# Optimization experiments

Hardware: AMD Instinct MI355X
Metric: run time of the kernel (lower is better)

## Reference

```python
import jax, jax.numpy as jnp
import numpy as np

SOFTCAP = 50.0
EPS = 1e-6
N_HEADS, D_HEAD = 16, 64


def _rms(x, w):
    return x * jax.lax.rsqrt(jnp.mean(x * x, axis=-1, keepdims=True) + EPS) * w


def _rope(x, cos, sin):
    # Faithful to source: apply_rope uses x.size(1) as the position axis, but is
    # called on (B, H, T, Dh) tensors, so positions are indexed by HEAD index.
    n = x.shape[1]
    x1, x2 = x[..., 0::2], x[..., 1::2]
    c = cos[:n][None, :, None, :]
    s = sin[:n][None, :, None, :]
    return jnp.stack([x1 * c - x2 * s, x1 * s + x2 * c], axis=-1).reshape(x.shape)


def setup_inputs() -> dict:
    key = jax.random.key(0)
    ks = jax.random.split(key, 12)
    L, D, H, Dh, Dff, V, B, T = 6, 1024, N_HEADS, D_HEAD, 4096, 32000, 1, 1024
    r = lambda k, shape: jax.random.normal(k, shape, dtype=jnp.float32) * 0.02
    return {
        'x': jax.random.randint(ks[0], (B, T), 0, V, dtype=jnp.int32),
        'embed': r(ks[1], (V, D)),
        'ln1': jnp.ones((L, D), jnp.float32),
        'Wq': r(ks[2], (L, H * Dh, D)),
        'Wk': r(ks[3], (L, H * Dh, D)),
        'Wv': r(ks[4], (L, H * Dh, D)),
        'Wo': r(ks[5], (L, D, H * Dh)),
        'qn': jnp.ones((L, Dh), jnp.float32),
        'kn': jnp.ones((L, Dh), jnp.float32),
        'ln2': jnp.ones((L, D), jnp.float32),
        'Wg': r(ks[6], (L, Dff, D)),
        'Wu': r(ks[7], (L, Dff, D)),
        'Wd': r(ks[8], (L, D, Dff)),
        'ln_out': jnp.ones((D,), jnp.float32),
    }


def reference(x, embed, ln1, Wq, Wk, Wv, Wo, qn, kn, ln2, Wg, Wu, Wd, ln_out):
    B, T = x.shape
    H, Dh = N_HEADS, D_HEAD
    scale = Dh ** -0.5
    # RoPE tables (theta=10000)
    freqs = 1.0 / (10000.0 ** (jnp.arange(0, Dh, 2, dtype=jnp.float32) / Dh))
    ang = jnp.arange(T, dtype=jnp.float32)[:, None] * freqs[None, :]
    cos, sin = jnp.cos(ang), jnp.sin(ang)
    mask = jnp.triu(jnp.ones((T, T), dtype=bool), k=1)  # True above diagonal

    h = embed[x]  # (B, T, D)

    def block(h, p):
        l1, wq, wk, wv, wo, qnw, knw, l2, wg, wu, wd = p
        hn = _rms(h, l1)
        q = (hn @ wq.T).reshape(B, T, H, Dh).transpose(0, 2, 1, 3)  # (B,H,T,Dh)
        k = (hn @ wk.T).reshape(B, T, H, Dh).transpose(0, 2, 1, 3)
        v = (hn @ wv.T).reshape(B, T, H, Dh).transpose(0, 2, 1, 3)
        q = _rope(_rms(q, qnw), cos, sin)
        k = _rope(_rms(k, knw), cos, sin)
        scores = jnp.einsum('bhtd,bhsd->bhts', q, k) * scale
        scores = SOFTCAP * jnp.tanh(scores / SOFTCAP)
        scores = jnp.where(mask[None, None], -jnp.inf, scores)
        attn = jax.nn.softmax(scores, axis=-1)
        o = jnp.einsum('bhts,bhsd->bhtd', attn, v)
        o = o.transpose(0, 2, 1, 3).reshape(B, T, H * Dh)
        h = h + o @ wo.T
        hn2 = _rms(h, l2)
        h = h + (jax.nn.silu(hn2 @ wg.T) * (hn2 @ wu.T)) @ wd.T
        return h, None

    h, _ = jax.lax.scan(block, h, (ln1, Wq, Wk, Wv, Wo, qn, kn, ln2, Wg, Wu, Wd))
    # tied embed/head
    logits = _rms(h, ln_out) @ embed.T  # (B, T, V)
    return logits
```

## Files before the change

kernel.cpp:

```cpp
#include <hip/hip_runtime.h>
#include <math.h>
#include <type_traits>

typedef __bf16 bf16_t;
typedef bf16_t bf16x4 __attribute__((ext_vector_type(4)));
typedef bf16_t bf16x8 __attribute__((ext_vector_type(8)));
typedef float  f32x4  __attribute__((ext_vector_type(4)));

#define RMS_EPS 1e-6f

enum { EP_STORE = 0, EP_RESID = 1, EP_SPLIT = 2, EP_SILU = 3, EP_QKV = 4 };

template<int V> using IC = std::integral_constant<int, V>;

static __device__ __forceinline__ f32x4 mfma16(bf16x8 a, bf16x8 b, f32x4 c) {
    return __builtin_amdgcn_mfma_f32_16x16x32_bf16(a, b, c, 0, 0, 0);
}

#define GLDS(gp, lp) __builtin_amdgcn_global_load_lds( \
    (const __attribute__((address_space(1))) void*)(gp), \
    (__attribute__((address_space(3))) void*)(lp), 16, 0, 0)

template<int N> static __device__ __forceinline__ void vmwait() {
    if constexpr (N == 0)      asm volatile("s_waitcnt vmcnt(0)" ::: "memory");
    else if constexpr (N == 2) asm volatile("s_waitcnt vmcnt(2)" ::: "memory");
    else if constexpr (N == 3) asm volatile("s_waitcnt vmcnt(3)" ::: "memory");
    else if constexpr (N == 4) asm volatile("s_waitcnt vmcnt(4)" ::: "memory");
    else if constexpr (N == 6) asm volatile("s_waitcnt vmcnt(6)" ::: "memory");
    else if constexpr (N == 8) asm volatile("s_waitcnt vmcnt(8)" ::: "memory");
    __builtin_amdgcn_sched_barrier(0);
}
static __device__ __forceinline__ void bar() { __builtin_amdgcn_s_barrier(); }
static __device__ __forceinline__ void lgkm0() {
    asm volatile("s_waitcnt lgkmcnt(0)" ::: "memory");
    __builtin_amdgcn_sched_barrier(0);
}

template<int BM, int BN, int WR, int WC, int PLANES, int EPIL, int MINW, int DEPTH>
__global__ __launch_bounds__(WR * WC * 64, MINW)
void gemm_bf16(const bf16_t* __restrict__ Ah, const bf16_t* __restrict__ Al,
               const bf16_t* __restrict__ Bh,
               float* __restrict__ Cf, bf16_t* __restrict__ Ch, bf16_t* __restrict__ Cl,
               int K, int lda, int ldb, int ldc, long long sC,
               const float* __restrict__ qnw, const float* __restrict__ knw)
{
    constexpr int ASZ = BM * 32, BSZ = BN * 32;
    constexpr int NW = WR * WC;
    constexpr int NLD = (BM / 16 * (PLANES >= 2 ? 2 : 1) + BN / 16) / NW;
    __shared__ __align__(16) bf16_t sAh[DEPTH][ASZ], sBh[DEPTH][BSZ];
    __shared__ __align__(16) bf16_t sAl[PLANES >= 2 ? DEPTH : 1][PLANES >= 2 ? ASZ : 8];

    const int gx = gridDim.x;
    int id = blockIdx.x + gx * blockIdx.y;
    if (gridDim.z == 1) {
        int nwg = gx * gridDim.y;
        int q = nwg >> 3, r = nwg & 7;
        int xcd = id & 7, ix = id >> 3;
        id = (xcd < r ? xcd * (q + 1) : r * (q + 1) + (xcd - r) * q) + ix;
    }
    const int bm = id % gx, bn = id / gx;
    const int row0 = bm * BM, col0 = bn * BN;

    const size_t kofs = (size_t)blockIdx.z * K;
    Ah += kofs;  Bh += kofs;
    if constexpr (PLANES >= 2) Al += kofs;

    const int tid = threadIdx.x, lane = tid & 63, wave = tid >> 6;
    const int lr = lane & 15, lg = lane >> 4;
    constexpr int WM = BM / WR, WN = BN / WC, MF = WM / 16, NF = WN / 16;
    const int wr = wave / WC, wc = wave % WC;

    f32x4 acc[MF][NF];
    #pragma unroll
    for (int m = 0; m < MF; ++m)
        #pragma unroll
        for (int n = 0; n < NF; ++n) acc[m][n] = (f32x4){0.f, 0.f, 0.f, 0.f};

    auto stage = [&](int k0, int p) {
        #pragma unroll
        for (int i = wave; i < BM / 16; i += NW) {
            int s = i * 64 + lane, rr = s >> 2, c = s & 3;
            size_t go = (size_t)(row0 + rr) * lda + k0 + ((c ^ ((rr >> 1) & 3)) << 3);
            GLDS(Ah + go, &sAh[p][i * 512]);
            if constexpr (PLANES >= 2) GLDS(Al + go, &sAl[p][i * 512]);
        }
        #pragma unroll
        for (int i = wave; i < BN / 16; i += NW) {
            int s = i * 64 + lane, rr = s >> 2, c = s & 3;
            size_t go = (size_t)(col0 + rr) * ldb + k0 + ((c ^ ((rr >> 1) & 3)) << 3);
            GLDS(Bh + go, &sBh[p][i * 512]);
        }
    };

    auto compute = [&](int p) {
        bf16x8 ahf[MF], alf[MF], bhf[NF];
        #pragma unroll
        for (int m = 0; m < MF; ++m) {
            int rr = wr * WM + m * 16 + lr;
            int by = rr * 64 + ((lg ^ ((rr >> 1) & 3)) << 4);
            ahf[m] = *(const bf16x8*)((const char*)&sAh[p][0] + by);
            if constexpr (PLANES >= 2)
                alf[m] = *(const bf16x8*)((const char*)&sAl[p][0] + by);
        }
        #pragma unroll
        for (int n = 0; n < NF; ++n) {
            int rr = wc * WN + n * 16 + lr;
            int by = rr * 64 + ((lg ^ ((rr >> 1) & 3)) << 4);
            bhf[n] = *(const bf16x8*)((const char*)&sBh[p][0] + by);
        }
        #pragma unroll
        for (int m = 0; m < MF; ++m)
            #pragma unroll
            for (int n = 0; n < NF; ++n) {
                acc[m][n] = mfma16(ahf[m], bhf[n], acc[m][n]);
                if constexpr (PLANES >= 2)
                    acc[m][n] = mfma16(alf[m], bhf[n], acc[m][n]);
            }
    };

    if constexpr (DEPTH == 3) {
        const int NC = K >> 5;
        stage(0, 0);
        stage(32, 1);
        for (int j = 0; j + 2 < NC; ++j) {
            stage(32 * (j + 2), (j + 2) % 3);
            vmwait<2 * NLD>(); bar();
            compute(j % 3);
            bar();
        }
        vmwait<NLD>(); bar();
        compute((K >> 5) >= 2 ? ((K >> 5) - 2) % 3 : 0);
        vmwait<0>(); bar();
        compute(((K >> 5) - 1) % 3);
    } else {
        stage(0, 0);
        int k0 = 32;
        for (; k0 + 32 < K; k0 += 64) {
            stage(k0, 1);
            vmwait<NLD>(); bar();
            compute(0);
            bar();
            stage(k0 + 32, 0);
            vmwait<NLD>(); bar();
            compute(1);
            bar();
        }
        stage(k0, 1);
        vmwait<NLD>(); bar();
        compute(0);
        bar();
        vmwait<0>(); bar();
        compute(1);
    }

    if constexpr (EPIL == EP_QKV) {
        const int colbase = col0 + wc * WN;
        const int typ = colbase >> 10;
        const float* nw = (typ == 0) ? qnw : knw;
        const int hh = (colbase - typ * 1024) >> 6;
        constexpr float kLogF = -0.41524101186092029f;
        #pragma unroll
        for (int m = 0; m < MF; ++m)
            #pragma unroll
            for (int r = 0; r < 4; ++r) {
                int grow = row0 + wr * WM + m * 16 + lg * 4 + r;
                if (typ < 2) {
                    float ss = 0.f;
                    #pragma unroll
                    for (int n = 0; n < NF; ++n) {
                        float v = acc[m][n][r];
                        ss += v * v;
                    }
                    ss += __shfl_xor(ss, 1, 64);
                    ss += __shfl_xor(ss, 2, 64);
                    ss += __shfl_xor(ss, 4, 64);
                    ss += __shfl_xor(ss, 8, 64);
                    float inv = rsqrtf(ss * (1.0f / 64.0f) + RMS_EPS);
                    #pragma unroll
                    for (int n = 0; n < NF; ++n) {
                        int i = n * 16 + lr;
                        float x = acc[m][n][r] * inv * nw[i];
                        float p = __shfl_xor(x, 1, 64);
                        float f = exp2f((float)(i >> 1) * kLogF);
                        float ang = (float)hh * f;
                        float cs = cosf(ang), sn = sinf(ang);
                        float o = (lr & 1) ? (p * sn + x * cs) : (x * cs - p * sn);
                        Ch[(size_t)grow * ldc + colbase + i] = (bf16_t)o;
                    }
                } else {
                    #pragma unroll
                    for (int n = 0; n < NF; ++n) {
                        float v = acc[m][n][r];
                        size_t off = (size_t)grow * ldc + colbase + n * 16 + lr;
                        bf16_t hb = (bf16_t)v;
                        Ch[off] = hb;
                        Cl[off] = (bf16_t)(v - (float)hb);
                    }
                }
            }
        return;
    }

    #pragma unroll
    for (int m = 0; m < MF; ++m)
        #pragma unroll
        for (int n = 0; n < NF; ++n)
            #pragma unroll
            for (int r = 0; r < 4; ++r) {
                int grow = row0 + wr * WM + m * 16 + lg * 4 + r;
                int gcol = col0 + wc * WN + n * 16 + lr;
                float v = acc[m][n][r];
                if constexpr (EPIL == EP_SILU) {
                    float pv = __shfl_xor(v, 1, 64);
                    if (!(lr & 1)) {
                        float s = (v / (1.0f + __expf(-v))) * pv;
                        size_t off = (size_t)grow * ldc + (gcol >> 1);
                        Ch[off] = (bf16_t)s;
                    }
                } else {
                    size_t off = (size_t)blockIdx.z * sC + (size_t)grow * ldc + gcol;
                    if constexpr (EPIL == EP_STORE) {
                        Cf[off] = v;
                    } else if constexpr (EPIL == EP_RESID) {
                        Cf[off] += v;
                    } else {
                        bf16_t hb = (bf16_t)v;
                        Ch[off] = hb;
                        Cl[off] = (bf16_t)(v - (float)hb);
                    }
                }
            }
}

__global__ __launch_bounds__(512, 2)
void gemm_logits8(const bf16_t* __restrict__ Ah, const bf16_t* __restrict__ Bh,
                  float* __restrict__ Cf)
{
    constexpr int lda = 1024, ldb = 1024, ldc = 32000;
    constexpr int NT = 16;
    __shared__ __align__(16) bf16_t sA[2][2][256 * 32];
    __shared__ __align__(16) bf16_t sB[2][2][256 * 32];

    const int gx = gridDim.x;
    int id = blockIdx.x + gx * blockIdx.y;
    {
        int nwg = gx * gridDim.y;
        int q = nwg >> 3, r = nwg & 7;
        int xcd = id & 7, ix = id >> 3;
        id = (xcd < r ? xcd * (q + 1) : r * (q + 1) + (xcd - r) * q) + ix;
    }
    const int bm = id % gx, bn = id / gx;
    const int row0 = bm * 256, col0 = bn * 256;

    const int tid = threadIdx.x, lane = tid & 63, wave = tid >> 6;
    const int lr = lane & 15, lg = lane >> 4;
    const int wr = wave >> 2, wc = wave & 3;

    f32x4 acc[8][4];
    #pragma unroll
    for (int m = 0; m < 8; ++m)
        #pragma unroll
        for (int n = 0; n < 4; ++n) acc[m][n] = (f32x4){0.f, 0.f, 0.f, 0.f};

    auto stageA = [&](int chunk, int buf, int ks) {
        int k0 = chunk * 32;
        #pragma unroll
        for (int i = wave; i < 16; i += 8) {
            int s = i * 64 + lane, rr = s >> 2, c = s & 3;
            size_t go = (size_t)(row0 + rr) * lda + k0 + ((c ^ ((rr >> 1) & 3)) << 3);
            GLDS(Ah + go, &sA[buf][ks][i * 512]);
        }
    };
    auto stageB = [&](int chunk, int buf, int ks) {
        int k0 = chunk * 32;
        #pragma unroll
        for (int i = wave; i < 16; i += 8) {
            int s = i * 64 + lane, rr = s >> 2, c = s & 3;
            size_t go = (size_t)(col0 + rr) * ldb + k0 + ((c ^ ((rr >> 1) & 3)) << 3);
            GLDS(Bh + go, &sB[buf][ks][i * 512]);
        }
    };

    auto phase = [&](int t, auto ksc) {
        constexpr int ks = decltype(ksc)::value;
        const int buf = t & 1;
        bf16x8 af[8], bf4[4];
        #pragma unroll
        for (int m = 0; m < 8; ++m) {
            int rr = wr * 128 + m * 16 + lr;
            int by = rr * 64 + ((lg ^ ((rr >> 1) & 3)) << 4);
            af[m] = *(const bf16x8*)((const char*)&sA[buf][ks][0] + by);
        }
        #pragma unroll
        for (int n = 0; n < 4; ++n) {
            int rr = wc * 64 + n * 16 + lr;
            int by = rr * 64 + ((lg ^ ((rr >> 1) & 3)) << 4);
            bf4[n] = *(const bf16x8*)((const char*)&sB[buf][ks][0] + by);
        }
        if constexpr (ks == 0) {
            if (t + 1 < NT) {
                stageA(2 * (t + 1) + 1, (t + 1) & 1, 1);
                stageB(2 * (t + 1) + 1, (t + 1) & 1, 1);
                vmwait<8>();
            } else {
                vmwait<0>();
            }
        } else {
            if (t + 2 < NT) {
                stageA(2 * (t + 2), t & 1, 0);
                stageB(2 * (t + 2), t & 1, 0);
                vmwait<8>();
            } else if (t + 1 < NT) {
                vmwait<4>();
            } else {
                vmwait<0>();
            }
        }
        bar();
        lgkm0();
        __builtin_amdgcn_s_setprio(1);
        #pragma unroll
        for (int m = 0; m < 8; ++m)
            #pragma unroll
            for (int n = 0; n < 4; ++n)
                acc[m][n] = mfma16(af[m], bf4[n], acc[m][n]);
        __builtin_amdgcn_s_setprio(0);
        bar();
    };

    stageA(0, 0, 0); stageB(0, 0, 0);
    stageA(1, 0, 1); stageB(1, 0, 1);
    stageA(2, 1, 0); stageB(2, 1, 0);
    vmwait<8>(); bar();

    for (int t = 0; t < NT; ++t) {
        phase(t, IC<0>{});
        phase(t, IC<1>{});
    }

    #pragma unroll
    for (int m = 0; m < 8; ++m)
        #pragma unroll
        for (int n = 0; n < 4; ++n)
            #pragma unroll
            for (int r = 0; r < 4; ++r) {
                int grow = row0 + wr * 128 + m * 16 + lg * 4 + r;
                int gcol = col0 + wc * 64 + n * 16 + lr;
                Cf[(size_t)grow * ldc + gcol] = acc[m][n][r];
            }
}

static __device__ __forceinline__ void wsplit_body(
    int b2, int tid,
    const float* wq, const float* wk, const float* wv, const float* wo,
    const float* wg, const float* wu, const float* wd,
    bf16_t* wAh, bf16_t* wGUh, bf16_t* wdh)
{
    #pragma unroll
    for (int k = 0; k < 4; ++k) {
        int b = b2 * 4 + k;
        const float* src;
        bf16_t* dst;
        size_t so, doff;
        if (b < 4096) {
            src = b < 1024 ? wq : b < 2048 ? wk : b < 3072 ? wv : wo;
            so = (size_t)(b & 1023) * 256 + tid;
            doff = (size_t)b * 256 + tid;
            dst = wAh;
        } else if (b < 12288) {
            int bb = b - 4096;
            int row = bb < 4096 ? 2 * bb : 2 * (bb - 4096) + 1;
            src = bb < 4096 ? wg : wu;
            so = (size_t)(bb & 4095) * 256 + tid;
            doff = (size_t)row * 256 + tid;
            dst = wGUh;
        } else {
            src = wd;
            so = (size_t)(b - 12288) * 256 + tid;
            doff = so;
            dst = wdh;
        }
        f32x4 v = ((const f32x4*)src)[so];
        bf16x4 hv;
        #pragma unroll
        for (int j = 0; j < 4; ++j) hv[j] = (bf16_t)v[j];
        ((bf16x4*)dst)[doff] = hv;
    }
}

__global__ __launch_bounds__(256)
void reduce_rms_wsplit(const float* __restrict__ p, float* __restrict__ h,
                       const float* __restrict__ w, bf16_t* __restrict__ outh,
                       const float* wq, const float* wk, const float* wv,
                       const float* wo, const float* wg, const float* wu,
                       const float* wd, bf16_t* wAh, bf16_t* wGUh, bf16_t* wdh)
{
    int blk = blockIdx.x, tid = threadIdx.x;
    if (blk >= 1024) {
        if (wq) wsplit_body(blk - 1024, tid, wq, wk, wv, wo, wg, wu, wd,
                            wAh, wGUh, wdh);
        return;
    }
    size_t i = (size_t)blk * 256 + tid;
    const size_t S = (1024 * 1024) / 4;
    f32x4 a = ((const f32x4*)p)[i];
    f32x4 b = ((const f32x4*)p)[i + S];
    f32x4 c = ((const f32x4*)p)[i + 2 * S];
    f32x4 d = ((const f32x4*)p)[i + 3 * S];
    f32x4 hv = ((const f32x4*)h)[i];
    #pragma unroll
    for (int j = 0; j < 4; ++j) hv[j] += (a[j] + b[j]) + (c[j] + d[j]);
    ((f32x4*)h)[i] = hv;

    float ss = hv[0]*hv[0] + hv[1]*hv[1] + hv[2]*hv[2] + hv[3]*hv[3];
    #pragma unroll
    for (int m = 1; m < 64; m <<= 1) ss += __shfl_xor(ss, m, 64);
    __shared__ float red[4];
    if ((tid & 63) == 0) red[tid >> 6] = ss;
    __syncthreads();
    float tot = red[0] + red[1] + red[2] + red[3];
    float inv = rsqrtf(tot * (1.0f / 1024.0f) + RMS_EPS);
    f32x4 wt4 = *(const f32x4*)(w + tid * 4);
    bf16x4 hv4;
    #pragma unroll
    for (int j = 0; j < 4; ++j) hv4[j] = (bf16_t)(hv[j] * inv * wt4[j]);
    ((bf16x4*)outh)[i] = hv4;
}

__global__ __launch_bounds__(256)
void gather_rms_wsplit(const int* __restrict__ ids, const float* __restrict__ embed,
                       const float* __restrict__ w, float* __restrict__ h,
                       bf16_t* __restrict__ outh,
                       const float* wq, const float* wk, const float* wv,
                       const float* wo, const float* wg, const float* wu,
                       const float* wd, bf16_t* wAh, bf16_t* wGUh, bf16_t* wdh)
{
    int blk = blockIdx.x, tid = threadIdx.x;
    if (blk >= 1024) {
        wsplit_body(blk - 1024, tid, wq, wk, wv, wo, wg, wu, wd, wAh, wGUh, wdh);
        return;
    }
    int row = ids[blk];
    f32x4 v = ((const f32x4*)(embed + (size_t)row * 1024))[tid];
    ((f32x4*)(h + (size_t)blk * 1024))[tid] = v;

    float ss = v[0]*v[0] + v[1]*v[1] + v[2]*v[2] + v[3]*v[3];
    #pragma unroll
    for (int m = 1; m < 64; m <<= 1) ss += __shfl_xor(ss, m, 64);
    __shared__ float red[4];
    if ((tid & 63) == 0) red[tid >> 6] = ss;
    __syncthreads();
    float tot = red[0] + red[1] + red[2] + red[3];
    float inv = rsqrtf(tot * (1.0f / 1024.0f) + RMS_EPS);
    f32x4 wt4 = *(const f32x4*)(w + tid * 4);
    bf16x4 hv;
    #pragma unroll
    for (int j = 0; j < 4; ++j) hv[j] = (bf16_t)(v[j] * inv * wt4[j]);
    ((bf16x4*)outh)[(size_t)blk * 256 + tid] = hv;
}

__global__ __launch_bounds__(128, 2)
void flash_attn(const bf16_t* __restrict__ qkvh,
                const bf16_t* __restrict__ vTh, const bf16_t* __restrict__ vTl,
                bf16_t* __restrict__ oh)
{
    __shared__ __align__(16) bf16_t sQ[32*64], sK[64*64], sVh[64*64], sVl[64*64];
    __shared__ __align__(16) bf16_t sPh[32*64], sPl[32*64];

    const int q0 = blockIdx.x * 32;
    const int hh = blockIdx.y;
    const int tid = threadIdx.x, lane = tid & 63, w = tid >> 6;
    const int lr = lane & 15, lg = lane >> 4;

    #pragma unroll
    for (int ii = 0; ii < 2; ++ii) {
        int r0 = w * 16 + ii * 8;
        int r  = r0 + (lane >> 3);
        int i  = lane & 7;
        GLDS(qkvh + (size_t)(q0 + r) * 3072 + hh * 64 + ((i ^ (r & 7)) << 3),
             sQ + r0 * 64);
    }
    __syncthreads();

    bf16x8 qa[2];
    #pragma unroll
    for (int ks = 0; ks < 2; ++ks) {
        int r = w * 16 + lr;
        qa[ks] = *(const bf16x8*)((const char*)sQ + r * 128 +
                                  ((((ks << 2) | lg) ^ (r & 7)) << 4));
    }

    f32x4 o_acc[4];
    #pragma unroll
    for (int n = 0; n < 4; ++n) o_acc[n] = (f32x4){0.f, 0.f, 0.f, 0.f};
    float m_run[4] = {-1e30f, -1e30f, -1e30f, -1e30f};
    float l_run[4] = {0.f, 0.f, 0.f, 0.f};

    const int ntiles = ((q0 + 31) >> 6) + 1;
    for (int t = 0; t < ntiles; ++t) {
        const int kv0 = t * 64;
        #pragma unroll
        for (int ii = 0; ii < 4; ++ii) {
            int r0 = w * 32 + ii * 8;
            int r  = r0 + (lane >> 3);
            int i  = lane & 7;
            GLDS(qkvh + (size_t)(kv0 + r) * 3072 + 1024 + hh * 64 + ((i ^ (r & 7)) << 3),
                 sK + r0 * 64);
            GLDS(vTh + (size_t)(hh * 64 + r) * 1024 + kv0 + ((i ^ (r & 7)) << 3),
                 sVh + r0 * 64);
            GLDS(vTl + (size_t)(hh * 64 + r) * 1024 + kv0 + ((i ^ (r & 7)) << 3),
                 sVl + r0 * 64);
        }
        __syncthreads();

        f32x4 s_acc[4];
        #pragma unroll
        for (int n = 0; n < 4; ++n) s_acc[n] = (f32x4){0.f, 0.f, 0.f, 0.f};
        #pragma unroll
        for (int ks = 0; ks < 2; ++ks)
            #pragma unroll
            for (int n = 0; n < 4; ++n) {
                int r = n * 16 + lr;
                bf16x8 kb = *(const bf16x8*)((const char*)sK + r * 128 +
                                             ((((ks << 2) | lg) ^ (r & 7)) << 4));
                s_acc[n] = mfma16(qa[ks], kb, s_acc[n]);
            }

        #pragma unroll
        for (int j = 0; j < 4; ++j) {
            int qr = q0 + w * 16 + lg * 4 + j;
            float p[4];
            float mx = -1e30f;
            #pragma unroll
            for (int n = 0; n < 4; ++n) {
                float sx = s_acc[n][j] * (0.125f * 0.02f);
                float v = 50.f * (1.f - 2.f / (1.f + __expf(2.f * sx)));
                int key = kv0 + n * 16 + lr;
                if (key > qr) v = -1e30f;
                p[n] = v;
                mx = fmaxf(mx, v);
            }
            #pragma unroll
            for (int m = 1; m < 16; m <<= 1) mx = fmaxf(mx, __shfl_xor(mx, m, 64));
            float mn = fmaxf(m_run[j], mx);
            float ef = __expf(m_run[j] - mn);
            m_run[j] = mn;
            float rs = 0.f;
            #pragma unroll
            for (int n = 0; n < 4; ++n) {
                float e = __expf(p[n] - mn);
                p[n] = e;
                rs += e;
            }
            #pragma unroll
            for (int m = 1; m < 16; m <<= 1) rs += __shfl_xor(rs, m, 64);
            l_run[j] = l_run[j] * ef + rs;
            #pragma unroll
            for (int n = 0; n < 4; ++n) o_acc[n][j] *= ef;
            int r = w * 16 + lg * 4 + j;
            #pragma unroll
            for (int n = 0; n < 4; ++n) {
                int c = n * 16 + lr;
                int byo = r * 128 + ((((c >> 3) ^ (r & 7)) << 4)) + ((c & 7) << 1);
                bf16_t hb = (bf16_t)p[n];
                *(bf16_t*)((char*)sPh + byo) = hb;
                *(bf16_t*)((char*)sPl + byo) = (bf16_t)(p[n] - (float)hb);
            }
        }

        #pragma unroll
        for (int ks = 0; ks < 2; ++ks) {
            int pr = w * 16 + lr;
            int pby = pr * 128 + ((((ks << 2) | lg) ^ (pr & 7)) << 4);
            bf16x8 pa  = *(const bf16x8*)((const char*)sPh + pby);
            bf16x8 pl_ = *(const bf16x8*)((const char*)sPl + pby);
            #pragma unroll
            for (int n = 0; n < 4; ++n) {
                int vr = n * 16 + lr;
                int vby = vr * 128 + ((((ks << 2) | lg) ^ (vr & 7)) << 4);
                bf16x8 vhf = *(const bf16x8*)((const char*)sVh + vby);
                bf16x8 vlf = *(const bf16x8*)((const char*)sVl + vby);
                o_acc[n] = mfma16(pa,  vhf, o_acc[n]);
                o_acc[n] = mfma16(pl_, vhf, o_acc[n]);
                o_acc[n] = mfma16(pa,  vlf, o_acc[n]);
            }
        }
        __syncthreads();
    }

    #pragma unroll
    for (int j = 0; j < 4; ++j) {
        float inv = 1.0f / l_run[j];
        int qr = q0 + w * 16 + lg * 4 + j;
        #pragma unroll
        for (int n = 0; n < 4; ++n) {
            size_t off = (size_t)qr * 1024 + hh * 64 + n * 16 + lr;
            oh[off] = (bf16_t)(o_acc[n][j] * inv);
        }
    }
}

__global__ __launch_bounds__(256)
void split_kernel(const float* __restrict__ src, bf16_t* __restrict__ hi)
{
    size_t i = (size_t)blockIdx.x * 256 + threadIdx.x;
    f32x4 v = ((const f32x4*)src)[i];
    bf16x4 hv;
    #pragma unroll
    for (int j = 0; j < 4; ++j) hv[j] = (bf16_t)v[j];
    ((bf16x4*)hi)[i] = hv;
}

__global__ __launch_bounds__(256)
void rmsnorm_split(const float* __restrict__ in, const float* __restrict__ w,
                   bf16_t* __restrict__ outh)
{
    int row = blockIdx.x, tid = threadIdx.x;
    f32x4 v = *(const f32x4*)(in + (size_t)row * 1024 + tid * 4);
    float ss = v[0]*v[0] + v[1]*v[1] + v[2]*v[2] + v[3]*v[3];
    #pragma unroll
    for (int m = 1; m < 64; m <<= 1) ss += __shfl_xor(ss, m, 64);
    __shared__ float red[4];
    if ((tid & 63) == 0) red[tid >> 6] = ss;
    __syncthreads();
    float tot = red[0] + red[1] + red[2] + red[3];
    float inv = rsqrtf(tot * (1.0f / 1024.0f) + RMS_EPS);
    f32x4 wt4 = *(const f32x4*)(w + tid * 4);
    bf16x4 hv;
    #pragma unroll
    for (int j = 0; j < 4; ++j) hv[j] = (bf16_t)(v[j] * inv * wt4[j]);
    ((bf16x4*)outh)[(size_t)row * 256 + tid] = hv;
}

__global__ __launch_bounds__(256)
void transpose_v(const bf16_t* __restrict__ qkvh, const bf16_t* __restrict__ qkvl,
                 bf16_t* __restrict__ vTh, bf16_t* __restrict__ vTl)
{
    __shared__ bf16_t tile[32][33];
    int b = blockIdx.x;
    int z = b >> 10, rem = b & 1023;
    const bf16_t* in = z ? qkvl : qkvh;
    bf16_t* out      = z ? vTl : vTh;
    int bx = (rem & 31) * 32, by = (rem >> 5) * 32;
    int r = threadIdx.x >> 5, c = threadIdx.x & 31;
    #pragma unroll
    for (int rr = r; rr < 32; rr += 8)
        tile[rr][c] = in[(size_t)(by + rr) * 3072 + 2048 + bx + c];
    __syncthreads();
    #pragma unroll
    for (int rr = r; rr < 32; rr += 8)
        out[(size_t)(bx + rr) * 1024 + by + c] = tile[c][rr];
}

extern "C" void kernel_launch(void* const* d_in, const int* in_sizes, int n_in,
                              void* d_out, int out_size, void* d_ws, size_t ws_size,
                              hipStream_t stream)
{
    (void)in_sizes; (void)n_in; (void)out_size; (void)ws_size;
    const int*   x_ids = (const int*)  d_in[0];
    const float* embed = (const float*)d_in[1];
    const float* ln1   = (const float*)d_in[2];
    const float* Wq    = (const float*)d_in[3];
    const float* Wk    = (const float*)d_in[4];
    const float* Wv    = (const float*)d_in[5];
    const float* Wo    = (const float*)d_in[6];
    const float* qn    = (const float*)d_in[7];
    const float* kn    = (const float*)d_in[8];
    const float* ln2   = (const float*)d_in[9];
    const float* Wg    = (const float*)d_in[10];
    const float* Wu    = (const float*)d_in[11];
    const float* Wd    = (const float*)d_in[12];
    const float* lnout = (const float*)d_in[13];
    float* out = (float*)d_out;

    char* ws = (char*)d_ws;
    const size_t MB = 1 << 20;
    float*  h    = (float*) (ws +   0 * MB);
    bf16_t* hnh  = (bf16_t*)(ws +   4 * MB);
    bf16_t* qkvh = (bf16_t*)(ws +   8 * MB);
    bf16_t* qkvl = (bf16_t*)(ws +  14 * MB);
    bf16_t* vTh  = (bf16_t*)(ws +  20 * MB);
    bf16_t* vTl  = (bf16_t*)(ws +  22 * MB);
    bf16_t* oh   = (bf16_t*)(ws +  24 * MB);
    bf16_t* wAh  = (bf16_t*)(ws +  28 * MB);
    bf16_t* wGUh = (bf16_t*)(ws +  36 * MB);
    bf16_t* wdh  = (bf16_t*)(ws +  52 * MB);
    bf16_t* silh = (bf16_t*)(ws +  60 * MB);
    float*  wdp  = (float*) (ws +  68 * MB);
    bf16_t* eh   = (bf16_t*)(ws +  84 * MB);

    const long long M1 = 1024 * 1024;

    gather_rms_wsplit<<<5120, 256, 0, stream>>>(
        x_ids, embed, ln1, h, hnh,
        Wq, Wk, Wv, Wo, Wg, Wu, Wd, wAh, wGUh, wdh);

    for (int l = 0; l < 6; ++l) {
        gemm_bf16<64,128,2,2,1,EP_QKV,4,3><<<dim3(16,24),256,0,stream>>>(
            hnh, nullptr, wAh, nullptr, qkvh, qkvl, 1024, 1024, 1024, 3072, 0,
            qn + l * 64, kn + l * 64);

        transpose_v<<<2048, 256, 0, stream>>>(qkvh, qkvl, vTh, vTl);

        flash_attn<<<dim3(32,16), 128, 0, stream>>>(qkvh, vTh, vTl, oh);

        gemm_bf16<64,64,2,2,1,EP_RESID,4,3><<<dim3(16,16),256,0,stream>>>(
            oh, nullptr, wAh + 3 * M1, h, nullptr, nullptr, 1024, 1024, 1024, 1024, 0,
            nullptr, nullptr);

        rmsnorm_split<<<1024, 256, 0, stream>>>(h, ln2 + l * 1024, hnh);

        gemm_bf16<128,256,2,4,1,EP_SILU,4,3><<<dim3(8,32),512,0,stream>>>(
            hnh, nullptr, wGUh, nullptr, silh, nullptr, 1024, 1024, 1024, 4096, 0,
            nullptr, nullptr);

        gemm_bf16<128,128,2,2,1,EP_STORE,4,3><<<dim3(8,8,4),256,0,stream>>>(
            silh, nullptr, wdh, wdp, nullptr, nullptr, 1024, 4096, 4096, 1024, M1,
            nullptr, nullptr);

        const float* wnext = (l < 5) ? (ln1 + (l + 1) * 1024) : lnout;
        if (l < 5) {
            reduce_rms_wsplit<<<5120, 256, 0, stream>>>(
                wdp, h, wnext, hnh,
                Wq + (size_t)(l+1) * M1, Wk + (size_t)(l+1) * M1,
                Wv + (size_t)(l+1) * M1, Wo + (size_t)(l+1) * M1,
                Wg + (size_t)(l+1) * 4 * M1, Wu + (size_t)(l+1) * 4 * M1,
                Wd + (size_t)(l+1) * 4 * M1, wAh, wGUh, wdh);
        } else {
            reduce_rms_wsplit<<<1024, 256, 0, stream>>>(
                wdp, h, wnext, hnh,
                nullptr, nullptr, nullptr, nullptr, nullptr, nullptr, nullptr,
                wAh, wGUh, wdh);
        }
    }

    split_kernel<<<32000, 256, 0, stream>>>(embed, eh);
    gemm_logits8<<<dim3(4,125), 512, 0, stream>>>(hnh, eh, out);
}
```

Before: 1.166 ms.

## Fuse V transpose into QKV GEMM epilogue and raise MFMA wave priority

The QKV GEMM epilogue now writes the V part straight into the transposed hi/lo bf16 buffers using 4-wide vector stores along the token dimension. This removes the separate transpose_v launch and its round trip through global memory, once per layer. It also wraps the MFMA loop in s_setprio so waves in the compute phase get issue priority over waves that are loading. The new transposed stores are strided by 1024 elements per column, so they may coalesce worse than the old row-wise writes.

```diff
diff --git a/kernel.cpp b/kernel.cpp
--- a/kernel.cpp
+++ b/kernel.cpp
@@ -108,6 +108,7 @@
             int by = rr * 64 + ((lg ^ ((rr >> 1) & 3)) << 4);
             bhf[n] = *(const bf16x8*)((const char*)&sBh[p][0] + by);
         }
+        __builtin_amdgcn_s_setprio(1);
         #pragma unroll
         for (int m = 0; m < MF; ++m)
             #pragma unroll
@@ -116,6 +117,7 @@
                 if constexpr (PLANES >= 2)
                     acc[m][n] = mfma16(alf[m], bhf[n], acc[m][n]);
             }
+        __builtin_amdgcn_s_setprio(0);
     };
 
     if constexpr (DEPTH == 3) {
@@ -156,15 +158,15 @@
     if constexpr (EPIL == EP_QKV) {
         const int colbase = col0 + wc * WN;
         const int typ = colbase >> 10;
-        const float* nw = (typ == 0) ? qnw : knw;
-        const int hh = (colbase - typ * 1024) >> 6;
-        constexpr float kLogF = -0.41524101186092029f;
-        #pragma unroll
-        for (int m = 0; m < MF; ++m)
-            #pragma unroll
-            for (int r = 0; r < 4; ++r) {
-                int grow = row0 + wr * WM + m * 16 + lg * 4 + r;
-                if (typ < 2) {
+        if (typ < 2) {
+            const float* nw = (typ == 0) ? qnw : knw;
+            const int hh = (colbase - typ * 1024) >> 6;
+            constexpr float kLogF = -0.41524101186092029f;
+            #pragma unroll
+            for (int m = 0; m < MF; ++m)
+                #pragma unroll
+                for (int r = 0; r < 4; ++r) {
+                    int grow = row0 + wr * WM + m * 16 + lg * 4 + r;
                     float ss = 0.f;
                     #pragma unroll
                     for (int n = 0; n < NF; ++n) {
@@ -187,17 +189,29 @@
                         float o = (lr & 1) ? (p * sn + x * cs) : (x * cs - p * sn);
                         Ch[(size_t)grow * ldc + colbase + i] = (bf16_t)o;
                     }
-                } else {
+                }
+        } else {
+            bf16_t* vTh_ = Cl;
+            bf16_t* vTl_ = (bf16_t*)Cf;
+            const int vcb = colbase - 2048;
+            #pragma unroll
+            for (int m = 0; m < MF; ++m)
+                #pragma unroll
+                for (int n = 0; n < NF; ++n) {
+                    int vc = vcb + n * 16 + lr;
+                    int grow0 = row0 + wr * WM + m * 16 + lg * 4;
+                    bf16x4 hv, lv;
                     #pragma unroll
-                    for (int n = 0; n < NF; ++n) {
+                    for (int r = 0; r < 4; ++r) {
                         float v = acc[m][n][r];
-                        size_t off = (size_t)grow * ldc + colbase + n * 16 + lr;
                         bf16_t hb = (bf16_t)v;
-                        Ch[off] = hb;
-                        Cl[off] = (bf16_t)(v - (float)hb);
+                        hv[r] = hb;
+                        lv[r] = (bf16_t)(v - (float)hb);
                     }
+                    *(bf16x4*)&vTh_[(size_t)vc * 1024 + grow0] = hv;
+                    *(bf16x4*)&vTl_[(size_t)vc * 1024 + grow0] = lv;
                 }
-            }
+        }
         return;
     }
 
@@ -632,26 +646,6 @@
     ((bf16x4*)outh)[(size_t)row * 256 + tid] = hv;
 }
 
-__global__ __launch_bounds__(256)
-void transpose_v(const bf16_t* __restrict__ qkvh, const bf16_t* __restrict__ qkvl,
-                 bf16_t* __restrict__ vTh, bf16_t* __restrict__ vTl)
-{
-    __shared__ bf16_t tile[32][33];
-    int b = blockIdx.x;
-    int z = b >> 10, rem = b & 1023;
-    const bf16_t* in = z ? qkvl : qkvh;
-    bf16_t* out      = z ? vTl : vTh;
-    int bx = (rem & 31) * 32, by = (rem >> 5) * 32;
-    int r = threadIdx.x >> 5, c = threadIdx.x & 31;
-    #pragma unroll
-    for (int rr = r; rr < 32; rr += 8)
-        tile[rr][c] = in[(size_t)(by + rr) * 3072 + 2048 + bx + c];
-    __syncthreads();
-    #pragma unroll
-    for (int rr = r; rr < 32; rr += 8)
-        out[(size_t)(bx + rr) * 1024 + by + c] = tile[c][rr];
-}
-
 extern "C" void kernel_launch(void* const* d_in, const int* in_sizes, int n_in,
                               void* d_out, int out_size, void* d_ws, size_t ws_size,
                               hipStream_t stream)
@@ -678,7 +672,6 @@
     float*  h    = (float*) (ws +   0 * MB);
     bf16_t* hnh  = (bf16_t*)(ws +   4 * MB);
     bf16_t* qkvh = (bf16_t*)(ws +   8 * MB);
-    bf16_t* qkvl = (bf16_t*)(ws +  14 * MB);
     bf16_t* vTh  = (bf16_t*)(ws +  20 * MB);
     bf16_t* vTl  = (bf16_t*)(ws +  22 * MB);
     bf16_t* oh   = (bf16_t*)(ws +  24 * MB);
@@ -697,10 +690,8 @@
 
     for (int l = 0; l < 6; ++l) {
         gemm_bf16<64,128,2,2,1,EP_QKV,4,3><<<dim3(16,24),256,0,stream>>>(
-            hnh, nullptr, wAh, nullptr, qkvh, qkvl, 1024, 1024, 1024, 3072, 0,
+            hnh, nullptr, wAh, (float*)vTl, qkvh, vTh, 1024, 1024, 1024, 3072, 0,
             qn + l * 64, kn + l * 64);
-
-        transpose_v<<<2048, 256, 0, stream>>>(qkvh, qkvl, vTh, vTl);
 
         flash_attn<<<dim3(32,16), 128, 0, stream>>>(qkvh, vTh, vTl, oh);
 
```

Measured after the change: 1.181 ms. Within noise of the previous version (+1.3%).
